# Kernel tuning notes

Measured on AMD Instinct MI355X. Metric: run time of the kernel, lower is better.

## Reference

```python
import jax, jax.numpy as jnp
import numpy as np

O, A, H, L = 32, 8, 256, 3   # obs_units, act_units, hidden_units, hidden_layers
SCALE = 1.0                  # obs_scale
N, W = 512, 128              # n obs/action rows, n hypernet weight samples
W_TOTAL = (O*H + H) + (A*H + H) + (2*H*H + H) + L*(H*H + H) + (H*O + O) + (H + 1) + (H + 1)  # 348194


def _unpack(w):
    # Slice the flat per-sample weight vector exactly as PrimaryNetwork.feedforward does.
    c = [0]
    def take(n, shape=None):
        s = w[:, c[0]:c[0]+n]
        c[0] += n
        return s.reshape((w.shape[0],) + shape) if shape is not None else s
    w_obs = take(O*H, (H, O)); b_obs = take(H)
    w_act = take(A*H, (H, A)); b_act = take(H)
    w_tgt = take(2*H*H, (H, 2*H)); b_tgt = take(H)
    ws, bs = [], []
    for _ in range(L):
        ws.append(take(H*H, (H, H))); bs.append(take(H))
    w_state = take(H*O, (O, H)); b_state = take(O)
    w_reward = take(H, (1, H)); b_reward = take(1)
    w_done = take(H, (1, H)); b_done = take(1)
    return w_obs, b_obs, w_act, b_act, w_tgt, b_tgt, ws, bs, w_state, b_state, w_reward, b_reward, w_done, b_done


def setup_inputs() -> dict:
    key = jax.random.key(0)
    k1, k2, k3 = jax.random.split(key, 3)
    return {
        "obs": jax.random.normal(k1, (N, O), jnp.float32),
        "action": jax.random.normal(k2, (N, A), jnp.float32),
        # scale ~1/sqrt(H) so activations stay in a sane range through the MLP
        "w": jax.random.normal(k3, (W, W_TOTAL), jnp.float32) * (1.0 / np.sqrt(H)),
        "obs_min": jnp.zeros((O,), jnp.float32),
        "obs_max": jnp.ones((O,), jnp.float32),
    }


def reference(obs, action, w, obs_min, obs_max):
    lrelu = jax.nn.leaky_relu  # negative_slope=0.01, matches F.leaky_relu default
    (w_obs, b_obs, w_act, b_act, w_tgt, b_tgt, ws, bs,
     w_state, b_state, w_reward, b_reward, w_done, b_done) = _unpack(w)

    # normalize obs to [-scale, scale]
    x = (obs - obs_min[None, :]) / (obs_max - obs_min)[None, :]
    x = (2.0 * x - 1.0) * SCALE                         # [N, O]

    # per-sample hypernetwork MLP, batched over (N obs rows) x (W weight samples)
    o = jnp.einsum('who,no->nwh', w_obs, x) + b_obs[None]          # [N, W, H]
    a = jnp.einsum('wha,na->nwh', w_act, action) + b_act[None]     # [N, W, H]
    y = lrelu(jnp.concatenate([o, a], axis=-1))                    # [N, W, 2H]
    y = lrelu(jnp.einsum('whk,nwk->nwh', w_tgt, y) + b_tgt[None])  # [N, W, H]
    for wj, bj in zip(ws, bs):
        y = lrelu(jnp.einsum('whk,nwk->nwh', wj, y) + bj[None])

    next_states = jnp.einsum('wok,nwk->nwo', w_state, y) + b_state[None] + x[:, None, :]  # [N, W, O]
    rewards = jnp.tanh(jnp.einsum('wok,nwk->nwo', w_reward, y) + b_reward[None])          # [N, W, 1]
    dones = jax.nn.sigmoid(jnp.einsum('wok,nwk->nwo', w_done, y) + b_done[None])          # [N, W, 1]

    # un-normalize next_states
    next_states = (next_states / SCALE + 1.0) * 0.5
    next_states = next_states * (obs_max - obs_min)[None, None, :] + obs_min[None, None, :]
    return next_states, rewards, dones
```

## Files before the change

### kernel.cpp

```cpp
#include <hip/hip_runtime.h>
#include <cstdint>
#include <cstddef>

#define NMEM    128
#define WTOTAL  348194

#define OFF_WOBS   0
#define OFF_BOBS   8192
#define OFF_WACT   8448
#define OFF_BACT   10496
#define OFF_WTGT   10752
#define OFF_BTGT   141824
#define OFF_WS0    142080
#define OFF_BS0    207616
#define OFF_WS1    207872
#define OFF_BS1    273408
#define OFF_WS2    273664
#define OFF_BS2    339200
#define OFF_WSTATE 339456
#define OFF_BSTATE 347648
#define OFF_WREW   347680
#define OFF_BREW   347936
#define OFF_WDONE  347937
#define OFF_BDONE  348193

#define OUT_REW  2097152
#define OUT_DONE 2162688

#define RB 128
#define APITCH 264

typedef __attribute__((ext_vector_type(8))) short short8;
typedef __attribute__((ext_vector_type(4))) float f32x4;

__device__ __forceinline__ uint32_t pkbf2(float lo, float hi) {
  union { float f; uint32_t u; } a, b;
  a.f = lo; b.f = hi;
  return __builtin_amdgcn_perm(b.u + 0x8000u, a.u + 0x8000u, 0x07060302u);
}

__device__ __forceinline__ uint16_t f2b_fast(float f) {
  union { float f; uint32_t u; } x; x.f = f;
  return (uint16_t)((x.u + 0x8000u) >> 16);
}

template <typename V, int NV>
__device__ __forceinline__ short8 pkT(const V g[NV]) {
  union { V v[NV]; float f[8]; } u;
#pragma unroll
  for (int i = 0; i < NV; ++i) u.v[i] = g[i];
  union { uint32_t u4[4]; short8 s; } r;
#pragma unroll
  for (int i = 0; i < 4; ++i) r.u4[i] = pkbf2(u.f[2 * i], u.f[2 * i + 1]);
  return r.s;
}

__device__ __forceinline__ short8 pk8f2(const float2 f[4]) {
  union { uint32_t u[4]; short8 s; } r;
#pragma unroll
  for (int i = 0; i < 4; ++i) r.u[i] = pkbf2(f[i].x, f[i].y);
  return r.s;
}

__device__ __forceinline__ void zero_acc(f32x4 a0[8], f32x4 a1[8]) {
#pragma unroll
  for (int r = 0; r < 8; ++r)
#pragma unroll
    for (int j = 0; j < 4; ++j) { a0[r][j] = 0.0f; a1[r][j] = 0.0f; }
}

template <typename V, int NV>
__device__ __forceinline__ void accum_pass(f32x4 acc0[8], f32x4 acc1[8],
                                           const uint16_t* __restrict__ Ab,
                                           const float* __restrict__ w0,
                                           const float* __restrict__ w1) {
  V g0[4][NV], g1[4][NV];
#pragma unroll
  for (int d = 0; d < 4; ++d) {
#pragma unroll
    for (int i = 0; i < NV; ++i) {
      g0[d][i] = reinterpret_cast<const V*>(w0 + d * 32)[i];
      g1[d][i] = reinterpret_cast<const V*>(w1 + d * 32)[i];
    }
  }
#pragma unroll
  for (int kt = 0; kt < 8; ++kt) {
    const int s = kt & 3;
    const short8 b0 = pkT<V, NV>(g0[s]);
    const short8 b1 = pkT<V, NV>(g1[s]);
    if (kt < 4) {
#pragma unroll
      for (int i = 0; i < NV; ++i) {
        g0[s][i] = reinterpret_cast<const V*>(w0 + (kt + 4) * 32)[i];
        g1[s][i] = reinterpret_cast<const V*>(w1 + (kt + 4) * 32)[i];
      }
    }
#pragma unroll
    for (int rt = 0; rt < 8; ++rt) {
      const short8 a =
          *reinterpret_cast<const short8*>(Ab + rt * 16 * APITCH + kt * 32);
      acc0[rt] = __builtin_amdgcn_mfma_f32_16x16x32_bf16(a, b0, acc0[rt], 0, 0, 0);
      acc1[rt] = __builtin_amdgcn_mfma_f32_16x16x32_bf16(a, b1, acc1[rt], 0, 0, 0);
    }
  }
}

__device__ __forceinline__ void epi2(const f32x4 acc0[8], const f32x4 acc1[8],
                                     float b0, float b1,
                                     uint16_t* __restrict__ B, int ct0, int ct1,
                                     int lg) {
#pragma unroll
  for (int rt = 0; rt < 8; ++rt) {
#pragma unroll
    for (int j = 0; j < 4; ++j) {
      const int row = rt * 16 + lg * 4 + j;
      float v0 = acc0[rt][j] + b0; v0 = (v0 > 0.0f) ? v0 : 0.01f * v0;
      float v1 = acc1[rt][j] + b1; v1 = (v1 > 0.0f) ? v1 : 0.01f * v1;
      B[row * APITCH + ct0] = f2b_fast(v0);
      B[row * APITCH + ct1] = f2b_fast(v1);
    }
  }
}

__global__ void __launch_bounds__(512, 2)
pn_kernel(const float* __restrict__ obs, const float* __restrict__ action,
          const float* __restrict__ w, const float* __restrict__ omin,
          const float* __restrict__ omax, float* __restrict__ out)
{
  __shared__ __align__(16) uint16_t B1[RB * APITCH];

  const int tid  = threadIdx.x;
  const int lane = tid & 63;
  const int wid  = tid >> 6;
  const int lr   = lane & 15;
  const int lg   = lane >> 4;
  const int ct0  = wid * 32 + lr;
  const int ct1  = ct0 + 16;

  const int bid    = blockIdx.x;
  const int xcd    = bid & 7;
  const int j5     = bid >> 3;
  const int member = xcd * 16 + (j5 >> 2);
  const int chunk  = j5 & 3;
  const int n0     = chunk * RB;
  const float* wm  = w + (size_t)member * WTOTAL;
  const bool al16  = ((member & 1) == 0);

  const uint16_t* Ab = B1 + lr * APITCH + lg * 8;

  f32x4 acc0[8], acc1[8];

  auto run_pass = [&](const float* w0, const float* w1) {
    if (al16) accum_pass<float4, 2>(acc0, acc1, Ab, w0, w1);
    else      accum_pass<float2, 4>(acc0, acc1, Ab, w0, w1);
  };

  {
    float sc[8], of[8];
#pragma unroll
    for (int i = 0; i < 8; ++i) {
      const float mn = omin[lg * 8 + i], mx = omax[lg * 8 + i];
      const float s = 2.0f / (mx - mn);
      sc[i] = s;
      of[i] = -mn * s - 1.0f;
    }
    float2 fb0[4], fb1[4];
#pragma unroll
    for (int i = 0; i < 4; ++i) {
      fb0[i] = reinterpret_cast<const float2*>(wm + OFF_WOBS + ct0 * 32 + lg * 8)[i];
      fb1[i] = reinterpret_cast<const float2*>(wm + OFF_WOBS + ct1 * 32 + lg * 8)[i];
    }
    const short8 b0 = pk8f2(fb0);
    const short8 b1 = pk8f2(fb1);
    const float bb0 = wm[OFF_BOBS + ct0], bb1 = wm[OFF_BOBS + ct1];
#pragma unroll
    for (int rt = 0; rt < 8; ++rt) {
      const int n = n0 + rt * 16 + lr;
      const float4 x0 = *reinterpret_cast<const float4*>(obs + n * 32 + lg * 8);
      const float4 x1 = *reinterpret_cast<const float4*>(obs + n * 32 + lg * 8 + 4);
      union { uint32_t u[4]; short8 s; } afr;
      afr.u[0] = pkbf2(x0.x * sc[0] + of[0], x0.y * sc[1] + of[1]);
      afr.u[1] = pkbf2(x0.z * sc[2] + of[2], x0.w * sc[3] + of[3]);
      afr.u[2] = pkbf2(x1.x * sc[4] + of[4], x1.y * sc[5] + of[5]);
      afr.u[3] = pkbf2(x1.z * sc[6] + of[6], x1.w * sc[7] + of[7]);
      f32x4 a0 = {0.0f, 0.0f, 0.0f, 0.0f}, a1 = {0.0f, 0.0f, 0.0f, 0.0f};
      a0 = __builtin_amdgcn_mfma_f32_16x16x32_bf16(afr.s, b0, a0, 0, 0, 0);
      a1 = __builtin_amdgcn_mfma_f32_16x16x32_bf16(afr.s, b1, a1, 0, 0, 0);
#pragma unroll
      for (int j = 0; j < 4; ++j) {
        float v0 = a0[j] + bb0; v0 = (v0 > 0.0f) ? v0 : 0.01f * v0;
        float v1 = a1[j] + bb1; v1 = (v1 > 0.0f) ? v1 : 0.01f * v1;
        B1[(rt * 16 + lg * 4 + j) * APITCH + ct0] = f2b_fast(v0);
        B1[(rt * 16 + lg * 4 + j) * APITCH + ct1] = f2b_fast(v1);
      }
    }
  }
  __syncthreads();

  zero_acc(acc0, acc1);

  run_pass(wm + OFF_WTGT + ct0 * 512 + lg * 8,
           wm + OFF_WTGT + ct1 * 512 + lg * 8);
  __syncthreads();

  {
    float2 fb0[4], fb1[4];
#pragma unroll
    for (int i = 0; i < 4; ++i) {
      fb0[i] = reinterpret_cast<const float2*>(wm + OFF_WACT + ct0 * 8 + lg * 8)[i];
      fb1[i] = reinterpret_cast<const float2*>(wm + OFF_WACT + ct1 * 8 + lg * 8)[i];
    }
    const short8 b0 = pk8f2(fb0);
    const short8 b1 = pk8f2(fb1);
    const float bb0 = wm[OFF_BACT + ct0], bb1 = wm[OFF_BACT + ct1];
#pragma unroll
    for (int rt = 0; rt < 8; ++rt) {
      const int n = n0 + rt * 16 + lr;
      union { uint32_t u[4]; short8 s; } afr;
      if (lg == 0) {
        const float4 q0 = *reinterpret_cast<const float4*>(action + n * 8);
        const float4 q1 = *reinterpret_cast<const float4*>(action + n * 8 + 4);
        afr.u[0] = pkbf2(q0.x, q0.y);
        afr.u[1] = pkbf2(q0.z, q0.w);
        afr.u[2] = pkbf2(q1.x, q1.y);
        afr.u[3] = pkbf2(q1.z, q1.w);
      } else {
        afr.u[0] = afr.u[1] = afr.u[2] = afr.u[3] = 0u;
      }
      f32x4 a0 = {0.0f, 0.0f, 0.0f, 0.0f}, a1 = {0.0f, 0.0f, 0.0f, 0.0f};
      a0 = __builtin_amdgcn_mfma_f32_16x16x32_bf16(afr.s, b0, a0, 0, 0, 0);
      a1 = __builtin_amdgcn_mfma_f32_16x16x32_bf16(afr.s, b1, a1, 0, 0, 0);
#pragma unroll
      for (int j = 0; j < 4; ++j) {
        float v0 = a0[j] + bb0; v0 = (v0 > 0.0f) ? v0 : 0.01f * v0;
        float v1 = a1[j] + bb1; v1 = (v1 > 0.0f) ? v1 : 0.01f * v1;
        B1[(rt * 16 + lg * 4 + j) * APITCH + ct0] = f2b_fast(v0);
        B1[(rt * 16 + lg * 4 + j) * APITCH + ct1] = f2b_fast(v1);
      }
    }
  }
  __syncthreads();

  run_pass(wm + OFF_WTGT + ct0 * 512 + 256 + lg * 8,
           wm + OFF_WTGT + ct1 * 512 + 256 + lg * 8);
  __syncthreads();
  epi2(acc0, acc1, wm[OFF_BTGT + ct0], wm[OFF_BTGT + ct1], B1, ct0, ct1, lg);
  __syncthreads();

  zero_acc(acc0, acc1);
  run_pass(wm + OFF_WS0 + ct0 * 256 + lg * 8, wm + OFF_WS0 + ct1 * 256 + lg * 8);
  __syncthreads();
  epi2(acc0, acc1, wm[OFF_BS0 + ct0], wm[OFF_BS0 + ct1], B1, ct0, ct1, lg);
  __syncthreads();

  zero_acc(acc0, acc1);
  run_pass(wm + OFF_WS1 + ct0 * 256 + lg * 8, wm + OFF_WS1 + ct1 * 256 + lg * 8);
  __syncthreads();
  epi2(acc0, acc1, wm[OFF_BS1 + ct0], wm[OFF_BS1 + ct1], B1, ct0, ct1, lg);
  __syncthreads();

  zero_acc(acc0, acc1);
  run_pass(wm + OFF_WS2 + ct0 * 256 + lg * 8, wm + OFF_WS2 + ct1 * 256 + lg * 8);
  __syncthreads();
  epi2(acc0, acc1, wm[OFF_BS2 + ct0], wm[OFF_BS2 + ct1], B1, ct0, ct1, lg);
  __syncthreads();

  if (wid < 2) {
    zero_acc(acc0, acc1);
#pragma unroll
    for (int kt = 0; kt < 8; ++kt) {
      short8 b0, b1;
      {
        union { uint32_t u[4]; short8 s; } z;
        z.u[0] = z.u[1] = z.u[2] = z.u[3] = 0u;
        b0 = z.s; b1 = z.s;
      }
      if (wid == 0) {
        float2 f0[4], f1[4];
#pragma unroll
        for (int i = 0; i < 4; ++i) {
          f0[i] = reinterpret_cast<const float2*>(
                      wm + OFF_WSTATE + ct0 * 256 + kt * 32 + lg * 8)[i];
          f1[i] = reinterpret_cast<const float2*>(
                      wm + OFF_WSTATE + ct1 * 256 + kt * 32 + lg * 8)[i];
        }
        b0 = pk8f2(f0);
        b1 = pk8f2(f1);
      } else if (lr == 0) {
        float2 f0[4];
#pragma unroll
        for (int i = 0; i < 4; ++i)
          f0[i] = reinterpret_cast<const float2*>(wm + OFF_WREW + kt * 32 + lg * 8)[i];
        b0 = pk8f2(f0);
      } else if (lr == 1) {
        const float* p = wm + OFF_WDONE + kt * 32 + lg * 8;
        union { uint32_t u[4]; short8 s; } r;
#pragma unroll
        for (int i = 0; i < 4; ++i) r.u[i] = pkbf2(p[2 * i], p[2 * i + 1]);
        b0 = r.s;
      }
#pragma unroll
      for (int rt = 0; rt < 8; ++rt) {
        const short8 a =
            *reinterpret_cast<const short8*>(Ab + rt * 16 * APITCH + kt * 32);
        acc0[rt] = __builtin_amdgcn_mfma_f32_16x16x32_bf16(a, b0, acc0[rt], 0, 0, 0);
        if (wid == 0)
          acc1[rt] = __builtin_amdgcn_mfma_f32_16x16x32_bf16(a, b1, acc1[rt], 0, 0, 0);
      }
    }

    if (wid == 0) {
      const float mn0 = omin[ct0], rg0 = omax[ct0] - mn0;
      const float mn1 = omin[ct1], rg1 = omax[ct1] - mn1;
      const float bs0 = wm[OFF_BSTATE + ct0], bs1 = wm[OFF_BSTATE + ct1];
#pragma unroll
      for (int rt = 0; rt < 8; ++rt) {
#pragma unroll
        for (int j = 0; j < 4; ++j) {
          const int n = n0 + rt * 16 + lg * 4 + j;
          const float x0 = 2.0f * (obs[n * 32 + ct0] - mn0) / rg0 - 1.0f;
          const float x1 = 2.0f * (obs[n * 32 + ct1] - mn1) / rg1 - 1.0f;
          float v0 = acc0[rt][j] + bs0 + x0;
          float v1 = acc1[rt][j] + bs1 + x1;
          v0 = (v0 + 1.0f) * 0.5f;
          v1 = (v1 + 1.0f) * 0.5f;
          out[((size_t)n * NMEM + member) * 32 + ct0] = v0 * rg0 + mn0;
          out[((size_t)n * NMEM + member) * 32 + ct1] = v1 * rg1 + mn1;
        }
      }
    } else {
      const float br = wm[OFF_BREW], bd = wm[OFF_BDONE];
#pragma unroll
      for (int rt = 0; rt < 8; ++rt) {
#pragma unroll
        for (int j = 0; j < 4; ++j) {
          const int n = n0 + rt * 16 + lg * 4 + j;
          if (lr == 0) {
            out[(size_t)OUT_REW + (size_t)n * NMEM + member] = tanhf(acc0[rt][j] + br);
          } else if (lr == 1) {
            out[(size_t)OUT_DONE + (size_t)n * NMEM + member] =
                1.0f / (1.0f + expf(-(acc0[rt][j] + bd)));
          }
        }
      }
    }
  }
}

extern "C" void kernel_launch(void* const* d_in, const int* in_sizes, int n_in,
                              void* d_out, int out_size, void* d_ws, size_t ws_size,
                              hipStream_t stream) {
  (void)in_sizes; (void)n_in; (void)out_size; (void)d_ws; (void)ws_size;
  const float* obs    = (const float*)d_in[0];
  const float* action = (const float*)d_in[1];
  const float* w      = (const float*)d_in[2];
  const float* omin   = (const float*)d_in[3];
  const float* omax   = (const float*)d_in[4];
  float* out = (float*)d_out;

  pn_kernel<<<dim3(512), dim3(512), 0, stream>>>(obs, action, w, omin, omax, out);
}
```

Measured before the change: 138.9 us.

## Prefetch next layer's weight slices across passes and drop float4 path

Each accumulation pass now loads the first four k-slices of the next layer's weights into registers while it consumes the last four slices of the current layer. Global weight-load latency at the start of each layer therefore overlaps the previous layer's MFMA work, the epilogue and the barriers. The first tgt slices and the action weights are also loaded before the obs stage. The alignment-dependent float4 variant is removed, so every pass uses float2 loads, which adds load instructions for even members. Keeping the prefetched registers live across barriers raises register pressure and could lower occupancy.

```diff
diff --git a/kernel.cpp b/kernel.cpp
--- a/kernel.cpp
+++ b/kernel.cpp
@@ -44,17 +44,6 @@
   return (uint16_t)((x.u + 0x8000u) >> 16);
 }
 
-template <typename V, int NV>
-__device__ __forceinline__ short8 pkT(const V g[NV]) {
-  union { V v[NV]; float f[8]; } u;
-#pragma unroll
-  for (int i = 0; i < NV; ++i) u.v[i] = g[i];
-  union { uint32_t u4[4]; short8 s; } r;
-#pragma unroll
-  for (int i = 0; i < 4; ++i) r.u4[i] = pkbf2(u.f[2 * i], u.f[2 * i + 1]);
-  return r.s;
-}
-
 __device__ __forceinline__ short8 pk8f2(const float2 f[4]) {
   union { uint32_t u[4]; short8 s; } r;
 #pragma unroll
@@ -69,30 +58,30 @@
     for (int j = 0; j < 4; ++j) { a0[r][j] = 0.0f; a1[r][j] = 0.0f; }
 }
 
-template <typename V, int NV>
+template <bool PF>
 __device__ __forceinline__ void accum_pass(f32x4 acc0[8], f32x4 acc1[8],
                                            const uint16_t* __restrict__ Ab,
                                            const float* __restrict__ w0,
-                                           const float* __restrict__ w1) {
-  V g0[4][NV], g1[4][NV];
-#pragma unroll
-  for (int d = 0; d < 4; ++d) {
-#pragma unroll
-    for (int i = 0; i < NV; ++i) {
-      g0[d][i] = reinterpret_cast<const V*>(w0 + d * 32)[i];
-      g1[d][i] = reinterpret_cast<const V*>(w1 + d * 32)[i];
-    }
-  }
+                                           const float* __restrict__ w1,
+                                           const float* __restrict__ nx0,
+                                           const float* __restrict__ nx1,
+                                           float2 g0[4][4], float2 g1[4][4]) {
 #pragma unroll
   for (int kt = 0; kt < 8; ++kt) {
     const int s = kt & 3;
-    const short8 b0 = pkT<V, NV>(g0[s]);
-    const short8 b1 = pkT<V, NV>(g1[s]);
+    const short8 b0 = pk8f2(g0[s]);
+    const short8 b1 = pk8f2(g1[s]);
     if (kt < 4) {
 #pragma unroll
-      for (int i = 0; i < NV; ++i) {
-        g0[s][i] = reinterpret_cast<const V*>(w0 + (kt + 4) * 32)[i];
-        g1[s][i] = reinterpret_cast<const V*>(w1 + (kt + 4) * 32)[i];
+      for (int i = 0; i < 4; ++i) {
+        g0[s][i] = reinterpret_cast<const float2*>(w0 + (kt + 4) * 32)[i];
+        g1[s][i] = reinterpret_cast<const float2*>(w1 + (kt + 4) * 32)[i];
+      }
+    } else if (PF) {
+#pragma unroll
+      for (int i = 0; i < 4; ++i) {
+        g0[s][i] = reinterpret_cast<const float2*>(nx0 + (kt - 4) * 32)[i];
+        g1[s][i] = reinterpret_cast<const float2*>(nx1 + (kt - 4) * 32)[i];
       }
     }
 #pragma unroll
@@ -144,16 +133,35 @@
   const int chunk  = j5 & 3;
   const int n0     = chunk * RB;
   const float* wm  = w + (size_t)member * WTOTAL;
-  const bool al16  = ((member & 1) == 0);
 
   const uint16_t* Ab = B1 + lr * APITCH + lg * 8;
 
-  f32x4 acc0[8], acc1[8];
-
-  auto run_pass = [&](const float* w0, const float* w1) {
-    if (al16) accum_pass<float4, 2>(acc0, acc1, Ab, w0, w1);
-    else      accum_pass<float2, 4>(acc0, acc1, Ab, w0, w1);
-  };
+  const float* wt0 = wm + OFF_WTGT + ct0 * 512 + lg * 8;
+  const float* wt1 = wm + OFF_WTGT + ct1 * 512 + lg * 8;
+  const float* wu0 = wt0 + 256;
+  const float* wu1 = wt1 + 256;
+  const float* wa0 = wm + OFF_WS0 + ct0 * 256 + lg * 8;
+  const float* wa1 = wm + OFF_WS0 + ct1 * 256 + lg * 8;
+  const float* wb0 = wm + OFF_WS1 + ct0 * 256 + lg * 8;
+  const float* wb1 = wm + OFF_WS1 + ct1 * 256 + lg * 8;
+  const float* wc0 = wm + OFF_WS2 + ct0 * 256 + lg * 8;
+  const float* wc1 = wm + OFF_WS2 + ct1 * 256 + lg * 8;
+
+  float2 g0[4][4], g1[4][4];
+#pragma unroll
+  for (int d = 0; d < 4; ++d) {
+#pragma unroll
+    for (int i = 0; i < 4; ++i) {
+      g0[d][i] = reinterpret_cast<const float2*>(wt0 + d * 32)[i];
+      g1[d][i] = reinterpret_cast<const float2*>(wt1 + d * 32)[i];
+    }
+  }
+  float2 fa0[4], fa1[4];
+#pragma unroll
+  for (int i = 0; i < 4; ++i) {
+    fa0[i] = reinterpret_cast<const float2*>(wm + OFF_WACT + ct0 * 8 + lg * 8)[i];
+    fa1[i] = reinterpret_cast<const float2*>(wm + OFF_WACT + ct1 * 8 + lg * 8)[i];
+  }
 
   {
     float sc[8], of[8];
@@ -197,21 +205,15 @@
   }
   __syncthreads();
 
+  f32x4 acc0[8], acc1[8];
   zero_acc(acc0, acc1);
 
-  run_pass(wm + OFF_WTGT + ct0 * 512 + lg * 8,
-           wm + OFF_WTGT + ct1 * 512 + lg * 8);
+  accum_pass<true>(acc0, acc1, Ab, wt0, wt1, wu0, wu1, g0, g1);
   __syncthreads();
 
   {
-    float2 fb0[4], fb1[4];
-#pragma unroll
-    for (int i = 0; i < 4; ++i) {
-      fb0[i] = reinterpret_cast<const float2*>(wm + OFF_WACT + ct0 * 8 + lg * 8)[i];
-      fb1[i] = reinterpret_cast<const float2*>(wm + OFF_WACT + ct1 * 8 + lg * 8)[i];
-    }
-    const short8 b0 = pk8f2(fb0);
-    const short8 b1 = pk8f2(fb1);
+    const short8 b0 = pk8f2(fa0);
+    const short8 b1 = pk8f2(fa1);
     const float bb0 = wm[OFF_BACT + ct0], bb1 = wm[OFF_BACT + ct1];
 #pragma unroll
     for (int rt = 0; rt < 8; ++rt) {
@@ -241,26 +243,25 @@
   }
   __syncthreads();
 
-  run_pass(wm + OFF_WTGT + ct0 * 512 + 256 + lg * 8,
-           wm + OFF_WTGT + ct1 * 512 + 256 + lg * 8);
+  accum_pass<true>(acc0, acc1, Ab, wu0, wu1, wa0, wa1, g0, g1);
   __syncthreads();
   epi2(acc0, acc1, wm[OFF_BTGT + ct0], wm[OFF_BTGT + ct1], B1, ct0, ct1, lg);
   __syncthreads();
 
   zero_acc(acc0, acc1);
-  run_pass(wm + OFF_WS0 + ct0 * 256 + lg * 8, wm + OFF_WS0 + ct1 * 256 + lg * 8);
+  accum_pass<true>(acc0, acc1, Ab, wa0, wa1, wb0, wb1, g0, g1);
   __syncthreads();
   epi2(acc0, acc1, wm[OFF_BS0 + ct0], wm[OFF_BS0 + ct1], B1, ct0, ct1, lg);
   __syncthreads();
 
   zero_acc(acc0, acc1);
-  run_pass(wm + OFF_WS1 + ct0 * 256 + lg * 8, wm + OFF_WS1 + ct1 * 256 + lg * 8);
+  accum_pass<true>(acc0, acc1, Ab, wb0, wb1, wc0, wc1, g0, g1);
   __syncthreads();
   epi2(acc0, acc1, wm[OFF_BS1 + ct0], wm[OFF_BS1 + ct1], B1, ct0, ct1, lg);
   __syncthreads();
 
   zero_acc(acc0, acc1);
-  run_pass(wm + OFF_WS2 + ct0 * 256 + lg * 8, wm + OFF_WS2 + ct1 * 256 + lg * 8);
+  accum_pass<false>(acc0, acc1, Ab, wc0, wc1, wc0, wc1, g0, g1);
   __syncthreads();
   epi2(acc0, acc1, wm[OFF_BS2 + ct0], wm[OFF_BS2 + ct1], B1, ct0, ct1, lg);
   __syncthreads();
```

Result: slower. 295.0 us (+112.3%).
